# Performance work log

Measured on AMD Instinct MI355X. Metric: run time of the kernel, lower is better.

The kernel has to match this reference:

```python
import jax, jax.numpy as jnp
import numpy as np
from jax import lax

# ---- model dims (match init_kwargs) ----
D = 2048        # hidden_size
HD = 128        # head_dim
HQ = 16         # num_q_heads (= expanded_num_heads)
HK = 8          # num_k_heads = num_v_heads
CONV = 4        # conv_size
CHUNK = 64      # chunk_size
NUM_ITER = 30   # chebyshev iterations
RIDGE = 0.02
EPS = 1e-6


def setup_inputs() -> dict:
    key = jax.random.key(0)
    ks = jax.random.split(key, 20)
    s = 0.02
    inp = {}
    inp['hidden_states'] = jax.random.normal(ks[0], (1, 1024, D), jnp.float32)
    inp['Wq'] = jax.random.normal(ks[1], (D, HQ * HD), jnp.float32) * s
    inp['Wk'] = jax.random.normal(ks[2], (D, HK * HD), jnp.float32) * s
    inp['Wv'] = jax.random.normal(ks[3], (D, HK * HD), jnp.float32) * s
    inp['conv_q'] = jax.random.normal(ks[4], (HQ * HD, CONV), jnp.float32) * 0.3
    inp['conv_k'] = jax.random.normal(ks[5], (HK * HD, CONV), jnp.float32) * 0.3
    inp['conv_v'] = jax.random.normal(ks[6], (HK * HD, CONV), jnp.float32) * 0.3
    inp['Wa'] = jax.random.normal(ks[7], (D, HQ), jnp.float32) * s
    # A_log = log(Uniform(0,16)) as in torch init
    inp['A_log'] = jnp.log(jax.random.uniform(ks[8], (HQ,), jnp.float32, 1e-3, 16.0))
    # dt_bias = inverse-softplus of dt ~ LogUniform(1e-3, 1e-1)
    dt = jnp.exp(jax.random.uniform(ks[9], (HQ,), jnp.float32) * (np.log(0.1) - np.log(0.001)) + np.log(0.001))
    dt = jnp.clip(dt, 1e-4, None)
    inp['dt_bias'] = dt + jnp.log(-jnp.expm1(-dt))
    inp['Wb'] = jax.random.normal(ks[10], (D, HQ), jnp.float32) * s
    inp['bb'] = jnp.zeros((HQ,), jnp.float32)
    inp['Walpha'] = jax.random.normal(ks[11], (D, HQ), jnp.float32) * s
    inp['balpha'] = jnp.zeros((HQ,), jnp.float32)
    inp['Wg'] = jax.random.normal(ks[12], (D, HQ * HD), jnp.float32) * s
    inp['norm_w'] = jnp.ones((HD,), jnp.float32)
    inp['Wo'] = jax.random.normal(ks[13], (HQ * HD, D), jnp.float32) * s
    return inp


def short_conv(x, w):
    # causal depthwise conv1d (kernel=CONV) + silu; x:[B,L,C], w:[C,K]
    K = w.shape[1]
    L = x.shape[1]
    xp = jnp.pad(x, ((0, 0), (K - 1, 0), (0, 0)))
    y = sum(xp[:, j:j + L, :] * w[:, j] for j in range(K))
    return jax.nn.silu(y)


def cheb_solve(A, b, lmin, lmax, num_iter):
    # Chebyshev semi-iteration for SPD A x = b, eigenvalue bounds [lmin, lmax].
    # A, b: [..., d, d]; lmin scalar; lmax: [..., 1, 1]
    theta = (lmax + lmin) / 2.0
    delta = (lmax - lmin) / 2.0
    sigma1 = theta / delta
    x = jnp.zeros_like(b)
    r = b
    rho = 1.0 / sigma1
    dvec = r / theta
    def body(carry, _):
        x, r, dvec, rho = carry
        x = x + dvec
        r = r - jnp.einsum('...de,...ef->...df', A, dvec)
        rho_n = 1.0 / (2.0 * sigma1 - rho)
        dvec = rho_n * rho * dvec + (2.0 * rho_n / delta) * r
        return (x, r, dvec, rho_n), None
    (x, _, _, _), _ = lax.scan(body, (x, r, dvec, rho), None, length=num_iter)
    return x


def reference(hidden_states, Wq, Wk, Wv, conv_q, conv_k, conv_v, Wa, A_log, dt_bias,
              Wb, bb, Walpha, balpha, Wg, norm_w, Wo):
    x = hidden_states
    B, L, _ = x.shape
    H, Hk, d, C = HQ, HK, HD, CHUNK
    Nc = L // C

    # projections + short causal convs with silu
    q = short_conv(x @ Wq, conv_q).reshape(B, L, H, d) * (d ** -0.5)  # gla rescale
    k = short_conv(x @ Wk, conv_k).reshape(B, L, Hk, d)
    v = short_conv(x @ Wv, conv_v).reshape(B, L, Hk, d)
    grp = H // Hk
    k = jnp.repeat(k, grp, axis=2)  # GQA expand: (h g) ordering
    v = jnp.repeat(v, grp, axis=2)

    # gates
    glog = -jnp.exp(A_log) * jax.nn.softplus(x @ Wa + dt_bias)   # [B,L,H], log forgetting gate <= 0
    beta = jax.nn.sigmoid(x @ Wb + bb)                           # [B,L,H]
    alpha = jax.nn.sigmoid(x @ Walpha + balpha)                  # [B,L,H]

    # chunk: [B,H,Nc,C,...]
    def ch(t):
        return t.reshape(B, Nc, C, H, -1).transpose(0, 3, 1, 2, 4)
    qc, kc, vc = ch(q), ch(k), ch(v)
    glc = glog.reshape(B, Nc, C, H).transpose(0, 3, 1, 2)   # [B,H,Nc,C]
    bc = beta.reshape(B, Nc, C, H).transpose(0, 3, 1, 2)

    cs = jnp.cumsum(glc, axis=-1)         # inclusive cumulative log-decay within chunk
    G = cs[..., -1]                        # total chunk decay [B,H,Nc]
    w_end = jnp.exp(G[..., None] - cs) * bc
    dHn = jnp.einsum('bhnc,bhncd,bhnce->bhnde', w_end, kc, kc)  # gram increment (forgetting_gate_kk)
    dBn = jnp.einsum('bhnc,bhncd,bhnce->bhnde', w_end, kc, vc)  # kv increment
    dg = jnp.exp(G)

    # inter-chunk state recurrence (scan over chunks)
    def step(carry, inp):
        Hs, Bs = carry
        g_n, dH_n, dB_n = inp
        out = (Hs, Bs)  # state at chunk START
        Hs = g_n[..., None, None] * Hs + dH_n
        Bs = g_n[..., None, None] * Bs + dB_n
        return (Hs, Bs), out
    init = (jnp.zeros((B, H, d, d), x.dtype), jnp.zeros((B, H, d, d), x.dtype))
    inputs = (dg.transpose(2, 0, 1), dHn.transpose(2, 0, 1, 3, 4), dBn.transpose(2, 0, 1, 3, 4))
    _, (H0, B0) = lax.scan(step, init, inputs)  # [Nc,B,H,d,d]

    # ridge-regularized Kalman solve per chunk via Chebyshev
    A = H0 + RIDGE * jnp.eye(d, dtype=x.dtype)
    lmax = jnp.trace(A, axis1=-2, axis2=-1)[..., None, None]  # trace >= lambda_max for SPD
    X = cheb_solve(A, B0, RIDGE, lmax, NUM_ITER)              # [Nc,B,H,d,d]
    Xc = X.transpose(1, 2, 0, 3, 4)                           # [B,H,Nc,d,d]

    # inter-chunk readout (through solved state)
    o_inter = jnp.exp(cs)[..., None] * jnp.einsum('bhncd,bhnde->bhnce', qc, Xc)
    # intra-chunk causal gated attention
    diff = cs[..., :, None] - cs[..., None, :]                # [B,H,Nc,C,C]
    mask = jnp.tril(jnp.ones((C, C), bool))
    dmat = jnp.exp(jnp.where(mask, diff, -1e30))
    scores = jnp.einsum('bhncd,bhnjd->bhncj', qc, kc) * dmat * bc[..., None, :]
    o_intra = jnp.einsum('bhncj,bhnjd->bhncd', scores, vc)

    o = (o_inter + o_intra).transpose(0, 2, 3, 1, 4).reshape(B, L, H, d)
    o = o + alpha[..., None] * v   # alpha connection (residual value path)

    # gated RMSNorm + output projection
    g_out = (x @ Wg).reshape(B, L, H, d)
    o = o * lax.rsqrt(jnp.mean(o * o, axis=-1, keepdims=True) + EPS) * norm_w
    o = o * jax.nn.silu(g_out)
    return o.reshape(B, L, H * d) @ Wo
```

## Files before the change

### kernel.cpp

```cpp
#include <hip/hip_runtime.h>
#include <math.h>


#define LSEQ 1024
#define DM   2048
#define NHQ  16
#define NHK  8
#define HDIM 128
#define NCH  16
#define CSZ  64

typedef __attribute__((ext_vector_type(8))) short short8;
typedef __attribute__((ext_vector_type(4))) float floatx4;

__device__ __forceinline__ unsigned short f2bf(float f) {
  unsigned int u = __float_as_uint(f);
  u += 0x7fffu + ((u >> 16) & 1u);
  return (unsigned short)(u >> 16);
}
__device__ __forceinline__ float bf2f(unsigned short u) {
  return __uint_as_float(((unsigned int)u) << 16);
}

__device__ __forceinline__ unsigned int cvtpk(float a, float b) {
  unsigned int r;
  asm("v_cvt_pk_bf16_f32 %0, %1, %2" : "=v"(r) : "v"(a), "v"(b));
  return r;
}

__device__ __forceinline__ void gload16(const unsigned short* g,
                                        unsigned short* l) {
  __builtin_amdgcn_global_load_lds(
      (const __attribute__((address_space(1))) unsigned int*)g,
      (__attribute__((address_space(3))) unsigned int*)l, 16, 0, 0);
}

__device__ __forceinline__ void tcast_fat(
    const float* __restrict__ W, unsigned short* __restrict__ Wt,
    int K, int N, int bn, int bk, int tid, float* __restrict__ t) {
  int k0 = bk * 128, n0 = bn * 64;
#pragma unroll
  for (int i = 0; i < 8; ++i) {
    int u = tid + i * 256;
    int r = u >> 4, c4 = u & 15;
    float4 v = *(const float4*)(W + (size_t)(k0 + r) * N + n0 + c4 * 4);
    float* dst = t + r * 65 + c4 * 4;
    dst[0] = v.x; dst[1] = v.y; dst[2] = v.z; dst[3] = v.w;
  }
  __syncthreads();
#pragma unroll
  for (int i = 0; i < 4; ++i) {
    int u2 = tid + i * 256;
    int klow = u2 & 7, nlow = (u2 >> 3) & 7;
    int khigh = (u2 >> 6) & 1, nhigh = (u2 >> 7) & 7;
    int k8 = (klow + khigh * 8) * 8;
    int nn = nlow + nhigh * 8;
    unsigned short o8[8];
#pragma unroll
    for (int j = 0; j < 8; ++j) o8[j] = f2bf(t[(k8 + j) * 65 + nn]);
    *(uint4*)(Wt + (size_t)(n0 + nn) * K + k0 + k8) = *(uint4*)o8;
  }
}

__global__ __launch_bounds__(256) void prep_kernel(
    const float* __restrict__ x, const float* __restrict__ Wq,
    const float* __restrict__ Wk, const float* __restrict__ Wv,
    const float* __restrict__ Wg, unsigned short* __restrict__ xb16,
    unsigned short* __restrict__ WtAll,
    const float* __restrict__ Wa, const float* __restrict__ Wbeta,
    const float* __restrict__ Wal, const float* __restrict__ A_log,
    const float* __restrict__ dtb, const float* __restrict__ bbv,
    const float* __restrict__ balv, float* __restrict__ glog,
    float* __restrict__ beta, float* __restrict__ alpha) {
  __shared__ float smem[128 * 65];
  int b = blockIdx.x, tid = threadIdx.x;
  if (b < 1024) {
    float* xr = smem;
    float* part = smem + 2048;
    int ts = b;
    for (int i = tid; i < 512; i += 256)
      ((float4*)xr)[i] = ((const float4*)(x + (size_t)ts * 2048))[i];
    __syncthreads();
    int o = tid >> 2, p = tid & 3;
    float s = 0.f;
    if (o < 48) {
      const float* W = (o < 16) ? Wa : (o < 32) ? Wbeta : Wal;
      int h = o & 15;
      int k0 = p * 512;
      for (int k = k0; k < k0 + 512; ++k) s = fmaf(xr[k], W[k * 16 + h], s);
    }
    part[tid] = s;
    __syncthreads();
    if (o < 48 && p == 0) {
      float dot = part[tid] + part[tid + 1] + part[tid + 2] + part[tid + 3];
      int h = o & 15;
      if (o < 16) {
        float za = dot + dtb[h];
        float sp = fmaxf(za, 0.f) + log1pf(expf(-fabsf(za)));
        glog[ts * 16 + h] = -expf(A_log[h]) * sp;
      } else if (o < 32) {
        beta[ts * 16 + h] = 1.f / (1.f + expf(-(dot + bbv[h])));
      } else {
        alpha[ts * 16 + h] = 1.f / (1.f + expf(-(dot + balv[h])));
      }
    }
  } else if (b < 2560) {
    int r = b - 1024;
    if (r < 512) {
      tcast_fat(Wq, WtAll, 2048, 2048, r & 31, r >> 5, tid, smem);
    } else if (r < 768) {
      int q = r - 512;
      tcast_fat(Wk, WtAll + (size_t)2048 * 2048, 2048, 1024, q & 15, q >> 4,
                tid, smem);
    } else if (r < 1024) {
      int q = r - 768;
      tcast_fat(Wv, WtAll + (size_t)3072 * 2048, 2048, 1024, q & 15, q >> 4,
                tid, smem);
    } else {
      int q = r - 1024;
      tcast_fat(Wg, WtAll + (size_t)4096 * 2048, 2048, 2048, q & 31, q >> 5,
                tid, smem);
    }
  } else {
    int i0 = (b - 2560) * 1024 + tid;
#pragma unroll
    for (int i = 0; i < 4; ++i) {
      int idx = i0 + i * 256;
      float4 v = ((const float4*)x)[idx];
      ushort4 u;
      u.x = f2bf(v.x); u.y = f2bf(v.y); u.z = f2bf(v.z); u.w = f2bf(v.w);
      ((ushort4*)xb16)[idx] = u;
    }
  }
}

template <int BM, int BN>
__global__ __launch_bounds__(256) void gemm_lds(
    const unsigned short* __restrict__ A, const unsigned short* __restrict__ Bt,
    float* __restrict__ C, int M, int N, int K) {
  __shared__ unsigned short As[BM * 64];
  __shared__ unsigned short Bs[BN * 64];
  constexpr int MT = BM / 32;
  constexpr int NT = BN / 32;
  constexpr int ACH = BM / 32;
  constexpr int BCH = BN / 32;
  int tid = threadIdx.x;
  int wave = tid >> 6, lane = tid & 63;
  int ln = lane & 15, hi = lane >> 4;
  int wm = wave & 1, wn = wave >> 1;
  int m0 = blockIdx.y * BM, n0 = blockIdx.x * BN;
  int lrow = lane >> 3, lcol = (lane & 7) * 8;

  floatx4 acc[MT][NT];
#pragma unroll
  for (int mt = 0; mt < MT; ++mt)
#pragma unroll
    for (int nt = 0; nt < NT; ++nt) acc[mt][nt] = (floatx4)(0.f);

  for (int k0 = 0; k0 < K; k0 += 64) {
#pragma unroll
    for (int i = 0; i < ACH; ++i) {
      int c = wave * ACH + i;
      gload16(A + (size_t)(m0 + c * 8 + lrow) * K + k0 + lcol, As + c * 512);
    }
#pragma unroll
    for (int i = 0; i < BCH; ++i) {
      int c = wave * BCH + i;
      gload16(Bt + (size_t)(n0 + c * 8 + lrow) * K + k0 + lcol, Bs + c * 512);
    }
    __syncthreads();
#pragma unroll
    for (int kb = 0; kb < 2; ++kb) {
      short8 a[MT], b[NT];
#pragma unroll
      for (int mt = 0; mt < MT; ++mt)
        a[mt] = *(const short8*)(As + (wm * (BM / 2) + mt * 16 + ln) * 64 +
                                 kb * 32 + hi * 8);
#pragma unroll
      for (int nt = 0; nt < NT; ++nt)
        b[nt] = *(const short8*)(Bs + (wn * (BN / 2) + nt * 16 + ln) * 64 +
                                 kb * 32 + hi * 8);
#pragma unroll
      for (int mt = 0; mt < MT; ++mt)
#pragma unroll
        for (int nt = 0; nt < NT; ++nt)
          acc[mt][nt] = __builtin_amdgcn_mfma_f32_16x16x32_bf16(
              a[mt], b[nt], acc[mt][nt], 0, 0, 0);
    }
    __syncthreads();
  }
#pragma unroll
  for (int mt = 0; mt < MT; ++mt)
#pragma unroll
    for (int nt = 0; nt < NT; ++nt) {
      int col = n0 + wn * (BN / 2) + nt * 16 + ln;
      int rowb = m0 + wm * (BM / 2) + mt * 16 + hi * 4;
#pragma unroll
      for (int r = 0; r < 4; ++r)
        C[(size_t)(rowb + r) * N + col] = acc[mt][nt][r];
    }
}

__device__ __forceinline__ float conv_core(
    const float* __restrict__ xin, const float* __restrict__ w,
    int idx, int instride, int nch, float scale) {
  int t = idx / nch, ch = idx - t * nch;
  float acc = 0.f;
#pragma unroll
  for (int j = 0; j < 4; ++j) {
    int tt = t + j - 3;
    float xv = (tt >= 0) ? xin[(size_t)tt * instride + ch] : 0.f;
    acc = fmaf(xv, w[ch * 4 + j], acc);
  }
  return acc / (1.f + expf(-acc)) * scale;
}

__global__ __launch_bounds__(256) void conv_all(
    const float* __restrict__ xall, const float* __restrict__ convq,
    const float* __restrict__ convk, const float* __restrict__ convv,
    unsigned short* __restrict__ qs16, float* __restrict__ ks2,
    unsigned short* __restrict__ ks16, float* __restrict__ vs2,
    const float* __restrict__ glog, const float* __restrict__ beta,
    float* __restrict__ cs, float* __restrict__ wend) {
  int b = blockIdx.x, tid = threadIdx.x;
  if (b < 8192) {
    int idx = b * 256 + tid;
    qs16[idx] = f2bf(conv_core(xall, convq, idx, 6144, 2048,
                               0.08838834764831845f));
  } else if (b < 12288) {
    int idx = (b - 8192) * 256 + tid;
    float v = conv_core(xall + 2048, convk, idx, 6144, 1024, 1.0f);
    ks2[idx] = v;
    ks16[idx] = f2bf(v);
  } else if (b < 16384) {
    int idx = (b - 12288) * 256 + tid;
    vs2[idx] = conv_core(xall + 3072, convv, idx, 6144, 1024, 1.0f);
  } else {
    int idx = tid;
    int n = idx & 15;
    float acc = 0.f;
    for (int c = 0; c < CSZ; ++c) {
      acc += glog[(n * CSZ + c) * NHQ + (idx >> 4)];
      cs[idx * CSZ + c] = acc;
    }
    float G = acc;
    for (int c = 0; c < CSZ; ++c) {
      wend[idx * CSZ + c] =
          expf(G - cs[idx * CSZ + c]) * beta[(n * CSZ + c) * NHQ + (idx >> 4)];
    }
  }
}

__global__ __launch_bounds__(256) void dhb_kernel(
    const float* __restrict__ ks, const float* __restrict__ vs,
    const float* __restrict__ wend, float* __restrict__ dH,
    float* __restrict__ dB, unsigned short* __restrict__ vT16) {
  __shared__ uint4 smem4[4096];
  int bid = blockIdx.x;
  int tid = threadIdx.x;

  if (bid >= 256) {
    float* t = (float*)smem4;
    int b = bid - 256;
    size_t gbase = ((size_t)(b >> 3)) * 65536 + ((size_t)(b & 7)) * 128;
#pragma unroll
    for (int g = 0; g < 8; ++g) {
      int i = tid + g * 256;
      int c = i >> 5, e4 = i & 31;
      float4 v = *(const float4*)(vs + gbase + (size_t)c * 1024 + e4 * 4);
      t[c * 132 + e4 * 4 + 0] = v.x;
      t[c * 132 + e4 * 4 + 1] = v.y;
      t[c * 132 + e4 * 4 + 2] = v.z;
      t[c * 132 + e4 * 4 + 3] = v.w;
    }
    __syncthreads();
    int e = tid >> 1, half = tid & 1;
    size_t obase = ((size_t)b << 13) + (size_t)e * 64 + half * 32;
#pragma unroll
    for (int cc = 0; cc < 8; ++cc) {
      int c0 = half * 32 + cc * 4;
      ushort4 u;
      u.x = f2bf(t[(c0 + 0) * 132 + e]);
      u.y = f2bf(t[(c0 + 1) * 132 + e]);
      u.z = f2bf(t[(c0 + 2) * 132 + e]);
      u.w = f2bf(t[(c0 + 3) * 132 + e]);
      *(ushort4*)(vT16 + obase + cc * 4) = u;
    }
    return;
  }

  unsigned short (*skF)[8192] = (unsigned short (*)[8192])smem4;
  unsigned short (*svF)[8192] =
      (unsigned short (*)[8192])((unsigned short*)smem4 + 16384);
  int h = bid >> 4, n = bid & 15;
  int hk = h >> 1;

#pragma unroll
  for (int p = 0; p < 4; ++p) {
    int t2 = tid + p * 256;
    int c0 = (t2 >> 7) << 3;
    int e = t2 & 127;
    int base = ((e >> 4) * 2 + (c0 >> 5)) * 512 +
               ((c0 & 31) >> 3) * 128 + (e & 15) * 8;
    unsigned short kh[8], kl[8], vh[8], vl[8];
#pragma unroll
    for (int j = 0; j < 8; ++j) {
      int c = c0 + j;
      float s = sqrtf(wend[bid * 64 + c]);
      size_t g = (size_t)(n * 64 + c) * 1024 + hk * 128 + e;
      float kf = s * ks[g];
      float vf = s * vs[g];
      unsigned short khh = f2bf(kf);
      kh[j] = khh; kl[j] = f2bf(kf - bf2f(khh));
      unsigned short vhh = f2bf(vf);
      vh[j] = vhh; vl[j] = f2bf(vf - bf2f(vhh));
    }
    *(uint4*)(&skF[0][base]) = *(uint4*)kh;
    *(uint4*)(&skF[1][base]) = *(uint4*)kl;
    *(uint4*)(&svF[0][base]) = *(uint4*)vh;
    *(uint4*)(&svF[1][base]) = *(uint4*)vl;
  }
  __syncthreads();

  int w = tid >> 6, lane = tid & 63;
  int ln = lane & 15, hi = lane >> 4;

  short8 ah[2][2], al[2][2];
#pragma unroll
  for (int mti = 0; mti < 2; ++mti) {
    int mt = w * 2 + mti;
#pragma unroll
    for (int ct = 0; ct < 2; ++ct) {
      ah[mti][ct] = *(const short8*)(&skF[0][((mt * 2 + ct) * 64 + lane) * 8]);
      al[mti][ct] = *(const short8*)(&skF[1][((mt * 2 + ct) * 64 + lane) * 8]);
    }
  }

  size_t gb = (size_t)bid << 14;
#pragma unroll
  for (int which = 0; which < 2; ++which) {
    const unsigned short (*BF)[8192] = which ? svF : skF;
    float* outp = which ? dB : dH;
#pragma unroll
    for (int nt = 0; nt < 8; ++nt) {
      floatx4 a0 = (floatx4)(0.f), a1 = (floatx4)(0.f);
#pragma unroll
      for (int ct = 0; ct < 2; ++ct) {
        short8 bh = *(const short8*)(&BF[0][((nt * 2 + ct) * 64 + lane) * 8]);
        short8 bl = *(const short8*)(&BF[1][((nt * 2 + ct) * 64 + lane) * 8]);
        a0 = __builtin_amdgcn_mfma_f32_16x16x32_bf16(ah[0][ct], bh, a0, 0, 0, 0);
        a0 = __builtin_amdgcn_mfma_f32_16x16x32_bf16(ah[0][ct], bl, a0, 0, 0, 0);
        a0 = __builtin_amdgcn_mfma_f32_16x16x32_bf16(al[0][ct], bh, a0, 0, 0, 0);
        a1 = __builtin_amdgcn_mfma_f32_16x16x32_bf16(ah[1][ct], bh, a1, 0, 0, 0);
        a1 = __builtin_amdgcn_mfma_f32_16x16x32_bf16(ah[1][ct], bl, a1, 0, 0, 0);
        a1 = __builtin_amdgcn_mfma_f32_16x16x32_bf16(al[1][ct], bh, a1, 0, 0, 0);
      }
      int e = nt * 16 + ln;
#pragma unroll
      for (int rg = 0; rg < 4; ++rg) {
        int d0 = (w * 2 + 0) * 16 + hi * 4 + rg;
        int d1 = (w * 2 + 1) * 16 + hi * 4 + rg;
        outp[gb + (size_t)d0 * 128 + e] = a0[rg];
        outp[gb + (size_t)d1 * 128 + e] = a1[rg];
      }
    }
  }
}

__global__ __launch_bounds__(256) void scan_kernel(
    float* __restrict__ dH, float* __restrict__ dB,
    const float* __restrict__ cs) {
  int idx = blockIdx.x * 256 + threadIdx.x;
  int h = idx >> 14, de = idx & 16383;
  float Hs = 0.f, Bs = 0.f;
  bool diag = ((de % 129) == 0);
#pragma unroll 1
  for (int n = 0; n < NCH; ++n) {
    size_t off = ((size_t)(h * 16 + n) << 14) + de;
    float dh = dH[off], db = dB[off];
    dH[off] = diag ? (Hs + 0.02f) : Hs;
    dB[off] = Bs;
    float g = expf(cs[(h * 16 + n) * CSZ + (CSZ - 1)]);
    Hs = fmaf(g, Hs, dh);
    Bs = fmaf(g, Bs, db);
  }
}

__global__ __launch_bounds__(256) void afrag_kernel(
    float* __restrict__ Aall, float* __restrict__ traces) {
  int bid = blockIdx.x;
  float* Ag = Aall + ((size_t)bid << 14);
  __shared__ float As[16384];
  int tid = threadIdx.x;
  for (int i = tid; i < 4096; i += 256)
    ((float4*)As)[i] = ((const float4*)Ag)[i];
  __syncthreads();
  if (tid < 64) {
    float tv = As[tid * 129] + As[(tid + 64) * 129];
#pragma unroll
    for (int off = 32; off; off >>= 1) tv += __shfl_down(tv, off);
    if (tid == 0) traces[bid] = tv;
  }
  unsigned short* Ah = (unsigned short*)Ag;
  unsigned short* Al = Ah + 16384;
#pragma unroll
  for (int c8 = 0; c8 < 8; ++c8) {
    int s0 = tid * 64 + c8 * 8;
    int frag = s0 >> 9, mlane = (s0 >> 3) & 63;
    int m = ((frag >> 2) << 4) + (mlane & 15);
    int k = ((frag & 3) << 5) + ((mlane >> 4) << 3);
    unsigned short hi[8], lo[8];
#pragma unroll
    for (int j = 0; j < 8; ++j) {
      float a = As[m * 128 + k + j];
      unsigned short h = f2bf(a);
      hi[j] = h;
      lo[j] = f2bf(a - bf2f(h));
    }
    *(uint4*)(Ah + s0) = *(uint4*)hi;
    *(uint4*)(Al + s0) = *(uint4*)lo;
  }
}

__global__ __launch_bounds__(256, 2) void cheb_kernel(
    const unsigned short* __restrict__ Afrag, const float* __restrict__ traces,
    float* __restrict__ Ball) {
  int bid = blockIdx.x;
  int bm = bid & 255;
  int cb = bid >> 8;
  const unsigned short* __restrict__ Ah = Afrag + ((size_t)bm << 15);
  float* __restrict__ Bg = Ball + ((size_t)bm << 14);
  __shared__ unsigned short dT[2][2048];
  int tid = threadIdx.x;
  int w = tid >> 6, lane = tid & 63;
  int ln = lane & 15, q = lane >> 4;

  float lmax = traces[bm];
  const float lmin = 0.02f;
  float theta = 0.5f * (lmax + lmin);
  float delta = 0.5f * (lmax - lmin);
  float sigma1 = theta / delta;
  float rho = delta / theta;
  float invtheta = 1.f / theta;

  short8 afr[2][4][2];
#pragma unroll
  for (int mt = 0; mt < 2; ++mt)
#pragma unroll
    for (int kt = 0; kt < 4; ++kt) {
      int f = (w * 2 + mt) * 4 + kt;
      afr[mt][kt][0] = *(const short8*)(Ah + ((f * 64 + lane) << 3));
      afr[mt][kt][1] = *(const short8*)(Ah + 16384 + ((f * 64 + lane) << 3));
    }

  int wrB[2];
#pragma unroll
  for (int mt = 0; mt < 2; ++mt)
    wrB[mt] = w * 512 + (((mt * 2 + (q >> 1)) & 3) * 16 + ln) * 8 +
              ((q & 1) << 2);

  float xx[2][4], rr[2][4], dd[2][4];
#pragma unroll
  for (int mt = 0; mt < 2; ++mt) {
#pragma unroll
    for (int rg = 0; rg < 4; ++rg) {
      float b = Bg[(w * 32 + mt * 16 + q * 4 + rg) * 128 + cb * 16 + ln];
      rr[mt][rg] = b;
      xx[mt][rg] = 0.f;
      dd[mt][rg] = b * invtheta;
    }
    unsigned int p01 = cvtpk(dd[mt][0], dd[mt][1]);
    unsigned int p23 = cvtpk(dd[mt][2], dd[mt][3]);
    dd[mt][0] = __uint_as_float(p01 << 16);
    dd[mt][1] = __uint_as_float(p01 & 0xffff0000u);
    dd[mt][2] = __uint_as_float(p23 << 16);
    dd[mt][3] = __uint_as_float(p23 & 0xffff0000u);
    uint2 pk; pk.x = p01; pk.y = p23;
    *(uint2*)(&dT[0][wrB[mt]]) = pk;
  }
  __syncthreads();

#pragma unroll 1
  for (int it = 0; it < 30; ++it) {
    const unsigned short* dTr = dT[it & 1];
    unsigned short* dTw = dT[(it & 1) ^ 1];
    floatx4 a0 = (floatx4)(0.f), a1 = (floatx4)(0.f);
#pragma unroll
    for (int kt = 0; kt < 4; ++kt) {
      short8 df = *(const short8*)(dTr + kt * 512 + lane * 8);
      a0 = __builtin_amdgcn_mfma_f32_16x16x32_bf16(afr[0][kt][0], df, a0, 0, 0, 0);
      a0 = __builtin_amdgcn_mfma_f32_16x16x32_bf16(afr[0][kt][1], df, a0, 0, 0, 0);
      a1 = __builtin_amdgcn_mfma_f32_16x16x32_bf16(afr[1][kt][0], df, a1, 0, 0, 0);
      a1 = __builtin_amdgcn_mfma_f32_16x16x32_bf16(afr[1][kt][1], df, a1, 0, 0, 0);
    }
    float rho_n = 1.f / (2.f * sigma1 - rho);
    float c1s = rho_n * rho;
    float c2s = 2.f * rho_n / delta;
#pragma unroll
    for (int mt = 0; mt < 2; ++mt) {
      float dn[4];
#pragma unroll
      for (int rg = 0; rg < 4; ++rg) {
        xx[mt][rg] += dd[mt][rg];
        rr[mt][rg] -= mt ? a1[rg] : a0[rg];
        dn[rg] = fmaf(c1s, dd[mt][rg], c2s * rr[mt][rg]);
      }
      unsigned int p01 = cvtpk(dn[0], dn[1]);
      unsigned int p23 = cvtpk(dn[2], dn[3]);
      dd[mt][0] = __uint_as_float(p01 << 16);
      dd[mt][1] = __uint_as_float(p01 & 0xffff0000u);
      dd[mt][2] = __uint_as_float(p23 << 16);
      dd[mt][3] = __uint_as_float(p23 & 0xffff0000u);
      uint2 pk; pk.x = p01; pk.y = p23;
      *(uint2*)(&dTw[wrB[mt]]) = pk;
    }
    rho = rho_n;
    __syncthreads();
  }

  unsigned short* Xf = (unsigned short*)Bg;
#pragma unroll
  for (int mt = 0; mt < 2; ++mt) {
    ushort4 h4, l4;
    unsigned short* hp = (unsigned short*)&h4;
    unsigned short* lp = (unsigned short*)&l4;
#pragma unroll
    for (int rg = 0; rg < 4; ++rg) {
      float xv = xx[mt][rg];
      unsigned short h = f2bf(xv);
      hp[rg] = h;
      lp[rg] = f2bf(xv - bf2f(h));
    }
    int lhi = wrB[mt];
    int llo = lhi + 2048;
    *(ushort4*)(Xf + ((lhi >> 5) << 8) + (cb << 5) + (lhi & 31)) = h4;
    *(ushort4*)(Xf + ((llo >> 5) << 8) + (cb << 5) + (llo & 31)) = l4;
  }
}

__global__ __launch_bounds__(256) void attn_kernel(
    const unsigned short* __restrict__ q16, const unsigned short* __restrict__ k16,
    const unsigned short* __restrict__ vT16, const unsigned short* __restrict__ Xf,
    const float* __restrict__ vs, const float* __restrict__ cs,
    const float* __restrict__ beta, const float* __restrict__ alpha,
    float* __restrict__ o) {
  int bid = blockIdx.x;
  int h = bid >> 4, n = bid & 15;
  int hk = h >> 1;
  __shared__ unsigned short qb[64 * 136];
  __shared__ unsigned short kb[64 * 136];
  __shared__ unsigned short Sb[64 * 72];
  __shared__ float csL[64], ecsL[64], betaL[64], alphaL[64];
  int tid = threadIdx.x;
  int w = tid >> 6, lane = tid & 63;
  int ln = lane & 15, hi = lane >> 4;

  {
    size_t qgb = (((size_t)(n * 64)) * 16 + h) * 128;
    size_t kgb = (((size_t)(n * 64)) * 8 + hk) * 128;
#pragma unroll
    for (int g = 0; g < 4; ++g) {
      int i = tid + g * 256;
      int c = i >> 4, ch = i & 15;
      *(uint4*)(qb + c * 136 + ch * 8) =
          *(const uint4*)(q16 + qgb + (size_t)c * 2048 + ch * 8);
      *(uint4*)(kb + c * 136 + ch * 8) =
          *(const uint4*)(k16 + kgb + (size_t)c * 1024 + ch * 8);
    }
    if (tid < 64) {
      float cv = cs[bid * 64 + tid];
      csL[tid] = cv;
      ecsL[tid] = expf(cv);
      betaL[tid] = beta[(n * 64 + tid) * 16 + h];
      alphaL[tid] = alpha[(n * 64 + tid) * 16 + h];
    }
  }
  __syncthreads();

  short8 aq[4];
#pragma unroll
  for (int dt = 0; dt < 4; ++dt)
    aq[dt] = *(const short8*)(qb + (w * 16 + ln) * 136 + dt * 32 + hi * 8);

  const unsigned short* Xb = Xf + ((size_t)bid << 15);
  floatx4 acc[8];
#pragma unroll
  for (int et = 0; et < 8; ++et) {
    floatx4 a = (floatx4)(0.f);
#pragma unroll
    for (int dt = 0; dt < 4; ++dt) {
      int base = ((dt * 16 + (lane >> 2)) << 8) + (et << 5) + ((lane & 3) << 3);
      short8 xh = *(const short8*)(Xb + base);
      short8 xl = *(const short8*)(Xb + base + 16384);
      a = __builtin_amdgcn_mfma_f32_16x16x32_bf16(aq[dt], xh, a, 0, 0, 0);
      a = __builtin_amdgcn_mfma_f32_16x16x32_bf16(aq[dt], xl, a, 0, 0, 0);
    }
    acc[et] = a;
  }
#pragma unroll
  for (int et = 0; et < 8; ++et)
#pragma unroll
    for (int rg = 0; rg < 4; ++rg)
      acc[et][rg] *= ecsL[w * 16 + hi * 4 + rg];

#pragma unroll
  for (int jt = 0; jt < 4; ++jt) {
    if (jt <= w) {
      floatx4 s = (floatx4)(0.f);
#pragma unroll
      for (int dt = 0; dt < 4; ++dt) {
        short8 bk = *(const short8*)(kb + (jt * 16 + ln) * 136 + dt * 32 + hi * 8);
        s = __builtin_amdgcn_mfma_f32_16x16x32_bf16(aq[dt], bk, s, 0, 0, 0);
      }
      int j = jt * 16 + ln;
      float csj = csL[j], bj = betaL[j];
#pragma unroll
      for (int rg = 0; rg < 4; ++rg) {
        int c = w * 16 + hi * 4 + rg;
        float v = (j <= c) ? s[rg] * expf(csL[c] - csj) * bj : 0.f;
        Sb[c * 72 + j] = f2bf(v);
      }
    } else {
#pragma unroll
      for (int rg = 0; rg < 4; ++rg)
        Sb[(w * 16 + hi * 4 + rg) * 72 + jt * 16 + ln] = 0;
    }
  }

  const unsigned short* vTb = vT16 + ((size_t)(n * 8 + hk) << 13);
#pragma unroll
  for (int et = 0; et < 8; ++et) {
#pragma unroll
    for (int kt = 0; kt < 2; ++kt) {
      short8 as = *(const short8*)(Sb + (w * 16 + ln) * 72 + kt * 32 + hi * 8);
      short8 bv = *(const short8*)(vTb + (et * 16 + ln) * 64 + kt * 32 + hi * 8);
      acc[et] = __builtin_amdgcn_mfma_f32_16x16x32_bf16(as, bv, acc[et], 0, 0, 0);
    }
  }

#pragma unroll
  for (int et = 0; et < 8; ++et) {
#pragma unroll
    for (int rg = 0; rg < 4; ++rg) {
      int c = w * 16 + hi * 4 + rg, e = et * 16 + ln;
      size_t oaddr = (((size_t)(n * 64 + c)) * 16 + h) * 128 + e;
      size_t vaddr = (((size_t)(n * 64 + c)) * 8 + hk) * 128 + e;
      o[oaddr] = acc[et][rg] + alphaL[c] * vs[vaddr];
    }
  }
}

__global__ __launch_bounds__(256) void rmso_kernel(
    const float* __restrict__ o, const float* __restrict__ xall,
    const float* __restrict__ norm_w, unsigned short* __restrict__ onorm,
    const float* __restrict__ Wo, unsigned short* __restrict__ WtWo) {
  __shared__ float t[128 * 65];
  int b = blockIdx.x, tid = threadIdx.x;
  if (b < 512) {
    tcast_fat(Wo, WtWo, 2048, 2048, b & 31, b >> 5, tid, t);
  } else {
    int bb = b - 512;
    int wave = tid >> 6, lane = tid & 63;
    int row = bb * 4 + wave;
    size_t base = (size_t)row * HDIM;
    size_t gbase = (size_t)(row >> 4) * 6144 + 4096 + (size_t)(row & 15) * HDIM;
    float v0 = o[base + lane], v1 = o[base + lane + 64];
    float ss = fmaf(v0, v0, v1 * v1);
#pragma unroll
    for (int off = 32; off; off >>= 1) ss += __shfl_down(ss, off);
    ss = __shfl(ss, 0);
    float rinv = rsqrtf(ss * (1.f / 128.f) + 1e-6f);
    float g0 = xall[gbase + lane], g1 = xall[gbase + lane + 64];
    float s0 = g0 / (1.f + expf(-g0));
    float s1 = g1 / (1.f + expf(-g1));
    onorm[base + lane]      = f2bf(v0 * rinv * norm_w[lane] * s0);
    onorm[base + lane + 64] = f2bf(v1 * rinv * norm_w[lane + 64] * s1);
  }
}

extern "C" void kernel_launch(void* const* d_in, const int* in_sizes, int n_in,
                              void* d_out, int out_size, void* d_ws,
                              size_t ws_size, hipStream_t stream) {
  (void)in_sizes; (void)n_in; (void)out_size; (void)ws_size;
  const float* x      = (const float*)d_in[0];
  const float* Wq     = (const float*)d_in[1];
  const float* Wk     = (const float*)d_in[2];
  const float* Wv     = (const float*)d_in[3];
  const float* convq  = (const float*)d_in[4];
  const float* convk  = (const float*)d_in[5];
  const float* convv  = (const float*)d_in[6];
  const float* Wa     = (const float*)d_in[7];
  const float* A_log  = (const float*)d_in[8];
  const float* dtb    = (const float*)d_in[9];
  const float* Wb     = (const float*)d_in[10];
  const float* bbv    = (const float*)d_in[11];
  const float* Wal    = (const float*)d_in[12];
  const float* balv   = (const float*)d_in[13];
  const float* Wg     = (const float*)d_in[14];
  const float* norm_w = (const float*)d_in[15];
  const float* Wo     = (const float*)d_in[16];
  float* out = (float*)d_out;

  float* p = (float*)d_ws;
  float* xall  = p; p += 6291456;
  float* qslot = p; p += 2097152;
  float* ks2   = p; p += 1048576;
  float* vs2   = p; p += 1048576;
  float* ob    = p; p += 2097152;
  float* glog  = p; p += 16384;
  float* beta  = p; p += 16384;
  float* alpha = p; p += 16384;
  float* csb   = p; p += 16384;
  float* wend  = p; p += 16384;
  float* traces= p; p += 16384;
  float* dHn   = p; p += 4194304;
  float* dBn   = p; p += 4194304;
  unsigned short* xb16 = (unsigned short*)p; p += 1048576;

  unsigned short* qs16 = (unsigned short*)qslot;
  unsigned short* ks16 = qs16 + 2097152;
  unsigned short* vT16 = ks16 + 1048576;
  unsigned short* WtAll = (unsigned short*)dHn;
  unsigned short* WtWo  = (unsigned short*)ks2;
  unsigned short* onorm16 = xb16;

  dim3 blk(256);
  prep_kernel<<<3072, blk, 0, stream>>>(x, Wq, Wk, Wv, Wg, xb16, WtAll,
                                        Wa, Wb, Wal, A_log, dtb, bbv, balv,
                                        glog, beta, alpha);
  gemm_lds<128, 64><<<dim3(96, 8), blk, 0, stream>>>(xb16, WtAll, xall,
                                                     1024, 6144, 2048);
  conv_all<<<16385, blk, 0, stream>>>(xall, convq, convk, convv,
                                      qs16, ks2, ks16, vs2,
                                      glog, beta, csb, wend);
  dhb_kernel<<<384, blk, 0, stream>>>(ks2, vs2, wend, dHn, dBn, vT16);
  scan_kernel<<<1024, blk, 0, stream>>>(dHn, dBn, csb);
  afrag_kernel<<<256, blk, 0, stream>>>(dHn, traces);
  cheb_kernel<<<2048, blk, 0, stream>>>((unsigned short*)dHn, traces, dBn);
  attn_kernel<<<256, blk, 0, stream>>>(qs16, ks16, vT16, (unsigned short*)dBn,
                                       vs2, csb, beta, alpha, ob);
  rmso_kernel<<<4608, blk, 0, stream>>>(ob, xall, norm_w, onorm16, Wo, WtWo);
  gemm_lds<64, 64><<<dim3(32, 16), blk, 0, stream>>>(onorm16, WtWo, out,
                                                     1024, 2048, 2048);
}
```

Baseline: 415.4 us.

## Split Chebyshev launch in two and move half of Wo transpose into attention kernel

The Chebyshev solve is now two launches of 1024 blocks, each covering half of the 256 matrices, where before it was one launch of 2048 blocks. The attention kernel gains 256 extra blocks that transpose and cast the first half of the Wo columns into the idle slots beside its 256 attention blocks. rmso keeps only the other half of that transpose. The goal is better use of the GPU during the small attention grid and shorter rmso work, at the cost of one extra kernel launch and a larger merged shared-memory footprint in attn_kernel.

```diff
diff --git a/kernel.cpp b/kernel.cpp
--- a/kernel.cpp
+++ b/kernel.cpp
@@ -424,10 +424,10 @@
 
 __global__ __launch_bounds__(256, 2) void cheb_kernel(
     const unsigned short* __restrict__ Afrag, const float* __restrict__ traces,
-    float* __restrict__ Ball) {
+    float* __restrict__ Ball, int bmoff) {
   int bid = blockIdx.x;
-  int bm = bid & 255;
-  int cb = bid >> 8;
+  int bm = (bid & 127) + bmoff;
+  int cb = bid >> 7;
   const unsigned short* __restrict__ Ah = Afrag + ((size_t)bm << 15);
   float* __restrict__ Bg = Ball + ((size_t)bm << 14);
   __shared__ unsigned short dT[2][2048];
@@ -543,15 +543,28 @@
     const unsigned short* __restrict__ vT16, const unsigned short* __restrict__ Xf,
     const float* __restrict__ vs, const float* __restrict__ cs,
     const float* __restrict__ beta, const float* __restrict__ alpha,
-    float* __restrict__ o) {
+    float* __restrict__ o, const float* __restrict__ Wo,
+    unsigned short* __restrict__ WtWo) {
+  __shared__ __align__(16) float smem[11264];
+  int tid = threadIdx.x;
+
+  if (blockIdx.x >= 256) {
+    int r = blockIdx.x - 256;
+    int bn = r & 15, bk = r >> 4;
+    tcast_fat(Wo, WtWo, 2048, 2048, bn, bk, tid, smem);
+    return;
+  }
+
   int bid = blockIdx.x;
   int h = bid >> 4, n = bid & 15;
   int hk = h >> 1;
-  __shared__ unsigned short qb[64 * 136];
-  __shared__ unsigned short kb[64 * 136];
-  __shared__ unsigned short Sb[64 * 72];
-  __shared__ float csL[64], ecsL[64], betaL[64], alphaL[64];
-  int tid = threadIdx.x;
+  unsigned short* qb = (unsigned short*)smem;
+  unsigned short* kb = qb + 8704;
+  unsigned short* Sb = kb + 8704;
+  float* csL = smem + 11008;
+  float* ecsL = csL + 64;
+  float* betaL = ecsL + 64;
+  float* alphaL = betaL + 64;
   int w = tid >> 6, lane = tid & 63;
   int ln = lane & 15, hi = lane >> 4;
 
@@ -656,10 +669,11 @@
     const float* __restrict__ Wo, unsigned short* __restrict__ WtWo) {
   __shared__ float t[128 * 65];
   int b = blockIdx.x, tid = threadIdx.x;
-  if (b < 512) {
-    tcast_fat(Wo, WtWo, 2048, 2048, b & 31, b >> 5, tid, t);
+  if (b < 256) {
+    int bn = 16 + (b & 15), bk = b >> 4;
+    tcast_fat(Wo, WtWo, 2048, 2048, bn, bk, tid, t);
   } else {
-    int bb = b - 512;
+    int bb = b - 256;
     int wave = tid >> 6, lane = tid & 63;
     int row = bb * 4 + wave;
     size_t base = (size_t)row * HDIM;
@@ -736,10 +750,11 @@
   dhb_kernel<<<384, blk, 0, stream>>>(ks2, vs2, wend, dHn, dBn, vT16);
   scan_kernel<<<1024, blk, 0, stream>>>(dHn, dBn, csb);
   afrag_kernel<<<256, blk, 0, stream>>>(dHn, traces);
-  cheb_kernel<<<2048, blk, 0, stream>>>((unsigned short*)dHn, traces, dBn);
-  attn_kernel<<<256, blk, 0, stream>>>(qs16, ks16, vT16, (unsigned short*)dBn,
-                                       vs2, csb, beta, alpha, ob);
-  rmso_kernel<<<4608, blk, 0, stream>>>(ob, xall, norm_w, onorm16, Wo, WtWo);
+  cheb_kernel<<<1024, blk, 0, stream>>>((unsigned short*)dHn, traces, dBn, 0);
+  cheb_kernel<<<1024, blk, 0, stream>>>((unsigned short*)dHn, traces, dBn, 128);
+  attn_kernel<<<512, blk, 0, stream>>>(qs16, ks16, vT16, (unsigned short*)dBn,
+                                       vs2, csb, beta, alpha, ob, Wo, WtWo);
+  rmso_kernel<<<4352, blk, 0, stream>>>(ob, xall, norm_w, onorm16, Wo, WtWo);
   gemm_lds<64, 64><<<dim3(32, 16), blk, 0, stream>>>(onorm16, WtWo, out,
                                                      1024, 2048, 2048);
 }
```

New measurement: 419.9 us. No clear change (+1.1%).
